# Kernel tuning notes

Measured on AMD Instinct MI355X. Metric: run time of the kernel, lower is better.

## Reference

```python
import jax, jax.numpy as jnp
import numpy as np


def _gat_layer(h, mask, w, a_src, a_dst):
    # h: [B,C,N,Fin], w: [C,H,Fin,Fout], a_*: [C,H,Fout,1], mask: [B,N,N] (True where no edge)
    h_prime = jnp.einsum('bcni,chio->bchno', h, w)          # [B,C,H,N,Fout]
    t = jnp.tanh(h_prime)
    s = jnp.einsum('bchno,cho->bchn', t, a_src[..., 0])      # src scores
    d = jnp.einsum('bchno,cho->bchn', t, a_dst[..., 0])      # dst scores
    attn = s[..., :, None] + d[..., None, :]                 # [B,C,H,N,N]
    attn = jnp.where(attn >= 0, attn, 0.2 * attn)            # leaky_relu(0.2)
    attn = jnp.where(mask[:, None, None, :, :], jnp.float32(-1e12), attn)
    attn = jax.nn.softmax(attn, axis=-1)
    return jnp.einsum('bchnm,bchmo->bchno', attn, h_prime)   # [B,C,H,N,Fout]


def setup_inputs() -> dict:
    key = jax.random.key(0)
    ks = jax.random.split(key, 8)
    B, C, N, F0, H, F = 2, 2, 1024, 64, 8, 64

    def xavier(k, shape):
        fan_in, fan_out = shape[-2], shape[-1]
        lim = (6.0 / (fan_in + fan_out)) ** 0.5
        return jax.random.uniform(k, shape, jnp.float32, -lim, lim)

    x = jax.random.normal(ks[0], (B, C, N, F0), dtype=jnp.float32)
    adj = jax.random.randint(ks[1], (B, N, N), 0, 2, dtype=jnp.int32)
    w1 = xavier(ks[2], (C, H, F0, F))
    a_src1 = xavier(ks[3], (C, H, F, 1))
    a_dst1 = xavier(ks[4], (C, H, F, 1))
    w2 = xavier(ks[5], (C, H, H * F, F))
    a_src2 = xavier(ks[6], (C, H, F, 1))
    a_dst2 = xavier(ks[7], (C, H, F, 1))
    return {"x": x, "adj": adj, "w1": w1, "a_src1": a_src1, "a_dst1": a_dst1,
            "w2": w2, "a_src2": a_src2, "a_dst2": a_dst2}


def reference(x, adj, w1, a_src1, a_dst1, w2, a_src2, a_dst2):
    B, C, N, _ = x.shape
    adj_f = adj.astype(jnp.float32) + jnp.eye(N, dtype=jnp.float32)[None]  # add self-loops
    mask = adj_f == 0                                        # [B,N,N]
    out1 = _gat_layer(x, mask, w1, a_src1, a_dst1)           # [B,C,H,N,F]
    # permute heads next to features, flatten, elu (dropout is identity in eval)
    x1 = jax.nn.elu(jnp.transpose(out1, (0, 1, 3, 2, 4)).reshape(B, C, N, -1))
    out2 = _gat_layer(x1, mask, w2, a_src2, a_dst2)          # [B,C,H,N,F]
    return out2.mean(axis=2)                                 # mean over heads -> [B,C,N,F]
```

## Files before the change

### kernel.cpp

```cpp
#include <hip/hip_runtime.h>

#define BB 2
#define CC 2
#define NN 1024
#define HH 8
#define BCHN 32
#define SVN  (BCHN*NN)
#define LOG2E 1.44269504f
#define X1S 520

typedef _Float16 f16x8 __attribute__((ext_vector_type(8)));
typedef _Float16 f16x4 __attribute__((ext_vector_type(4)));
typedef __fp16 h16x2 __attribute__((ext_vector_type(2)));
typedef float f32x4 __attribute__((ext_vector_type(4)));

__device__ __forceinline__ float fexp2(float x) {
  float r; asm("v_exp_f32 %0, %1" : "=v"(r) : "v"(x)); return r;
}


__global__ __launch_bounds__(256) void proj1_fused(
    const float* __restrict__ x, const int* __restrict__ adj,
    const float* __restrict__ w1, const float* __restrict__ w2,
    const float* __restrict__ asrc, const float* __restrict__ adst,
    _Float16* __restrict__ w2T, unsigned long long* __restrict__ bmg,
    _Float16* __restrict__ HpT, float* __restrict__ s_out, float* __restrict__ d_out)
{
  __shared__ union {
    __align__(16) _Float16 tile[64*72];
    struct { float sp[4][32]; float sd[4][32]; } pr;
  } sm;
  const int bx = blockIdx.x;
  const int t = threadIdx.x;
  const int w = t >> 6, lane = t & 63;
  const int colr = lane & 15, quad = lane >> 4;

  if (bx < 1024) {
    const int bch = bx & 31;
    const int row0 = (bx >> 5) * 32;
    const int h = bch & 7; const int bc = bch >> 3; const int c = bc & 1;

    const float* Ar0 = x + ((size_t)bc*NN + row0 + colr)*64;
    const float* Ar1 = Ar0 + (size_t)16*64;
    const float* Bw  = w1 + ((size_t)(c*HH + h))*64*64 + w*16 + colr;

    f32x4 acc0 = {0.f,0.f,0.f,0.f}, acc1 = {0.f,0.f,0.f,0.f};
    #pragma unroll
    for (int kb = 0; kb < 64; kb += 32) {
      const float4 pa0 = *(const float4*)(Ar0 + kb + quad*8);
      const float4 pa1 = *(const float4*)(Ar0 + kb + quad*8 + 4);
      const float4 pb0 = *(const float4*)(Ar1 + kb + quad*8);
      const float4 pb1 = *(const float4*)(Ar1 + kb + quad*8 + 4);
      float bv[8];
      #pragma unroll
      for (int j = 0; j < 8; ++j) bv[j] = Bw[(size_t)(kb + quad*8 + j)*64];
      f16x8 a0, a1, bf;
      a0[0]=(_Float16)pa0.x; a0[1]=(_Float16)pa0.y; a0[2]=(_Float16)pa0.z; a0[3]=(_Float16)pa0.w;
      a0[4]=(_Float16)pa1.x; a0[5]=(_Float16)pa1.y; a0[6]=(_Float16)pa1.z; a0[7]=(_Float16)pa1.w;
      a1[0]=(_Float16)pb0.x; a1[1]=(_Float16)pb0.y; a1[2]=(_Float16)pb0.z; a1[3]=(_Float16)pb0.w;
      a1[4]=(_Float16)pb1.x; a1[5]=(_Float16)pb1.y; a1[6]=(_Float16)pb1.z; a1[7]=(_Float16)pb1.w;
      #pragma unroll
      for (int j = 0; j < 8; ++j) bf[j] = (_Float16)bv[j];
      acc0 = __builtin_amdgcn_mfma_f32_16x16x32_f16(a0, bf, acc0, 0, 0, 0);
      acc1 = __builtin_amdgcn_mfma_f32_16x16x32_f16(a1, bf, acc1, 0, 0, 0);
    }

    const float af  = asrc[(c*HH + h)*64 + w*16 + colr];
    const float bf_ = adst[(c*HH + h)*64 + w*16 + colr];
    _Float16* HT = HpT + (size_t)bch*65536 + (size_t)(row0 >> 5)*2048
                       + (size_t)(w*16 + colr)*32;

    #pragma unroll
    for (int mt = 0; mt < 2; ++mt) {
      const f32x4 a = mt ? acc1 : acc0;
      f16x4 hv;
      #pragma unroll
      for (int i = 0; i < 4; ++i) {
        const float v = a[i];
        hv[i] = (_Float16)v;
        const float ex = __expf(2.f*v);
        const float th = 1.f - 2.f/(ex + 1.f);
        float ps = th * af, pd = th * bf_;
        #pragma unroll
        for (int off = 1; off < 16; off <<= 1) {
          ps += __shfl_xor(ps, off);
          pd += __shfl_xor(pd, off);
        }
        if (colr == 0) {
          sm.pr.sp[w][mt*16 + quad*4 + i] = ps;
          sm.pr.sd[w][mt*16 + quad*4 + i] = pd;
        }
      }
      *(f16x4*)(HT + mt*16 + quad*4) = hv;
    }
    __syncthreads();
    if (t < 32) {
      const float sv = sm.pr.sp[0][t] + sm.pr.sp[1][t] + sm.pr.sp[2][t] + sm.pr.sp[3][t];
      const float dv = sm.pr.sd[0][t] + sm.pr.sd[1][t] + sm.pr.sd[2][t] + sm.pr.sd[3][t];
      s_out[bch*NN + row0 + t] = sv * LOG2E;
      d_out[bch*NN + row0 + t] = dv * LOG2E;
    }
  } else if (bx < 1152) {
    const int u = bx - 1024;
    const int ch = u >> 3, k0 = (u & 7)*64;
    const float* src = w2 + ((size_t)ch*512 + k0)*64;
    #pragma unroll
    for (int j = 0; j < 4; ++j) {
      const int uu = t + j*256;
      const int k = uu >> 4, seg = uu & 15;
      const float4 v = ((const float4*)src)[(size_t)k*16 + seg];
      sm.tile[(seg*4+0)*72 + k] = (_Float16)v.x;
      sm.tile[(seg*4+1)*72 + k] = (_Float16)v.y;
      sm.tile[(seg*4+2)*72 + k] = (_Float16)v.z;
      sm.tile[(seg*4+3)*72 + k] = (_Float16)v.w;
    }
    __syncthreads();
    _Float16* dst = w2T + (size_t)ch*32768;
    #pragma unroll
    for (int j = 0; j < 2; ++j) {
      const int uu = t + j*256;
      const int f = uu >> 3, seg = uu & 7;
      const f16x8 o = *(const f16x8*)&sm.tile[f*72 + seg*8];
      const int kk = k0 + seg*8;
      *(f16x8*)(dst + (size_t)(kk >> 5)*2048 + (size_t)f*32 + (kk & 31)) = o;
    }
  } else {
    const int g = (bx - 1152)*4 + w;
    const int base = g*32;
    #pragma unroll
    for (int jb = 0; jb < 4; ++jb) {
      int vals[8];
      #pragma unroll
      for (int i = 0; i < 8; ++i) {
        const int idx = base + jb*8 + i;
        const int b = idx >> 14;
        const int n = (idx >> 4) & (NN - 1);
        const int wd = idx & 15;
        vals[i] = adj[((size_t)b*NN + n)*NN + wd*64 + lane];
      }
      #pragma unroll
      for (int i = 0; i < 8; ++i) {
        const int idx = base + jb*8 + i;
        const int n = (idx >> 4) & (NN - 1);
        const int m = (idx & 15)*64 + lane;
        const unsigned long long bits = __ballot((vals[i] != 0) || (m == n));
        if (lane == 0) bmg[idx] = bits;
      }
    }
  }
}

template<int LAYER>
__global__ __launch_bounds__(1024, 4) void attn_monster(
    const _Float16* __restrict__ HpTin, const float* __restrict__ s_arr,
    const float* __restrict__ d_arr, const unsigned long long* __restrict__ bmg,
    const _Float16* __restrict__ w2T, const float* __restrict__ asrc2,
    const float* __restrict__ adst2,
    _Float16* __restrict__ HpT2, float* __restrict__ s2, float* __restrict__ d2,
    float* __restrict__ out)
{
  __shared__ union {
    struct {
      float obuf[8][16][68];
      float dsb[8][16];
      float spb[8][16];
      float sdb[8][16];
      __align__(16) _Float16 x1[16*X1S];
    } l1;
    struct { float mbuf[16][64]; float dsb[8][16]; } l2;
  } sm;

  const int bc = blockIdx.x;
  const int r0 = blockIdx.y * 16;
  const int t = threadIdx.x;
  const int wv = t >> 6;
  const int h  = wv >> 1, kh = wv & 1;
  const int lane = t & 63;
  const int colr = lane & 15, quad = lane >> 4;
  const int bch = bc*HH + h;
  const int b = bc >> 1, c = bc & 1;

  if (LAYER == 2) sm.l2.mbuf[t >> 6][t & 63] = 0.f;
  else if (t < 256) (&sm.l1.spb[0][0])[t] = 0.f;

  const float* dg = d_arr + (size_t)bch*NN;
  const float4* dg4 = (const float4*)dg;
  float mxl = -1e30f;
  #pragma unroll
  for (int j = 0; j < 4; ++j) {
    const float4 v = dg4[lane + 64*j];
    mxl = fmaxf(fmaxf(v.x, v.y), fmaxf(fmaxf(v.z, v.w), mxl));
  }
  #pragma unroll
  for (int off = 1; off < 64; off <<= 1) mxl = fmaxf(mxl, __shfl_xor(mxl, off));
  const float maxd = mxl;

  const int r = r0 + colr;
  const float s = s_arr[(size_t)bch*NN + r];
  const float so = s + maxd;
  const float offs = fmaxf(so, 0.2f*so);
  const float sA = s - offs, sB = 0.2f*s - offs;

  unsigned long long m[8];
  {
    const unsigned long long* bm = bmg + ((size_t)b*NN + r)*16 + kh*8;
    #pragma unroll
    for (int j = 0; j < 8; ++j) m[j] = bm[j];
  }

  const _Float16* Bp = HpTin + (size_t)bch*65536 + (size_t)kh*32768 + quad*8;
  const float* dgk = dg + kh*512 + quad*8;

  f32x4 acc[4];
  f32x4 accs = {0.f,0.f,0.f,0.f};
  #pragma unroll
  for (int ft = 0; ft < 4; ++ft) acc[ft] = (f32x4){0.f,0.f,0.f,0.f};
  f16x8 ones;
  #pragma unroll
  for (int i = 0; i < 8; ++i) ones[i] = (_Float16)1.f;

  f16x8 B0[4], B1[4];
  #pragma unroll
  for (int ft = 0; ft < 4; ++ft) B0[ft] = *(const f16x8*)(Bp + (ft*16 + colr)*32);
  #pragma unroll
  for (int ft = 0; ft < 4; ++ft) B1[ft] = *(const f16x8*)(Bp + 2048 + (ft*16 + colr)*32);
  float4 dc0 = *(const float4*)(dgk),      dc1 = *(const float4*)(dgk + 4);
  float4 dn0 = *(const float4*)(dgk + 32), dn1 = *(const float4*)(dgk + 36);

  #pragma unroll
  for (int ks = 0; ks < 16; ++ks) {
    const unsigned mb = (unsigned)((m[ks >> 1] >> ((ks & 1)*32 + quad*8)) & 0xFFull);
    const float dd[8] = {dc0.x, dc0.y, dc0.z, dc0.w, dc1.x, dc1.y, dc1.z, dc1.w};
    union { f16x8 v; h16x2 hh[4]; } A;
    #pragma unroll
    for (int jp = 0; jp < 4; ++jp) {
      float p[2];
      #pragma unroll
      for (int jj = 0; jj < 2; ++jj) {
        const int j = jp*2 + jj;
        const float dj = dd[j];
        const float l = fmaxf(sA + dj, fmaf(0.2f, dj, sB));
        p[jj] = ((mb >> j) & 1u) ? fexp2(l) : 0.f;
      }
      A.hh[jp] = __builtin_amdgcn_cvt_pkrtz(p[0], p[1]);
    }
    #pragma unroll
    for (int ft = 0; ft < 4; ++ft)
      acc[ft] = __builtin_amdgcn_mfma_f32_16x16x32_f16(A.v, B0[ft], acc[ft], 0, 0, 0);
    accs = __builtin_amdgcn_mfma_f32_16x16x32_f16(A.v, ones, accs, 0, 0, 0);
    #pragma unroll
    for (int ft = 0; ft < 4; ++ft) B0[ft] = B1[ft];
    dc0 = dn0; dc1 = dn1;
    if (ks < 14) {
      #pragma unroll
      for (int ft = 0; ft < 4; ++ft)
        B1[ft] = *(const f16x8*)(Bp + (size_t)(ks+2)*2048 + (ft*16 + colr)*32);
      dn0 = *(const float4*)(dgk + (ks+2)*32);
      dn1 = *(const float4*)(dgk + (ks+2)*32 + 4);
    }
  }

  if (LAYER == 1) {
    if (kh == 0) {
      #pragma unroll
      for (int ft = 0; ft < 4; ++ft)
        #pragma unroll
        for (int i = 0; i < 4; ++i)
          sm.l1.obuf[h][quad*4 + i][ft*16 + colr] = acc[ft][i];
      if (colr == 0) {
        #pragma unroll
        for (int i = 0; i < 4; ++i) sm.l1.dsb[h][quad*4 + i] = accs[i];
      }
    }
    __syncthreads();
    if (kh == 1) {
      #pragma unroll
      for (int ft = 0; ft < 4; ++ft)
        #pragma unroll
        for (int i = 0; i < 4; ++i)
          sm.l1.obuf[h][quad*4 + i][ft*16 + colr] += acc[ft][i];
      if (colr == 0) {
        #pragma unroll
        for (int i = 0; i < 4; ++i) sm.l1.dsb[h][quad*4 + i] += accs[i];
      }
    }
    __syncthreads();
    {
      const int row = t >> 6;
      const int hp  = (t >> 3) & 7;
      const int f0  = (t & 7)*8;
      const float invd = 1.f / sm.l1.dsb[hp][row];
      const float* ob = &sm.l1.obuf[hp][row][f0];
      f16x8 xo;
      #pragma unroll
      for (int j = 0; j < 8; ++j) {
        float v = ob[j] * invd;
        v = v > 0.f ? v : expm1f(v);
        xo[j] = (_Float16)v;
      }
      *(f16x8*)&sm.l1.x1[row*X1S + hp*64 + f0] = xo;
    }
    __syncthreads();

    const int fb = kh*2;
    const _Float16* Bw = w2T + (size_t)(c*HH + h)*32768 + quad*8;
    f32x4 acc2[2];
    acc2[0] = (f32x4){0.f,0.f,0.f,0.f}; acc2[1] = (f32x4){0.f,0.f,0.f,0.f};
    f16x8 Wc[2], Wn[2];
    #pragma unroll
    for (int u = 0; u < 2; ++u) Wc[u] = *(const f16x8*)(Bw + ((fb+u)*16 + colr)*32);
    #pragma unroll
    for (int u = 0; u < 2; ++u) Wn[u] = *(const f16x8*)(Bw + 2048 + ((fb+u)*16 + colr)*32);
    #pragma unroll
    for (int k2 = 0; k2 < 16; ++k2) {
      const f16x8 Af = *(const f16x8*)&sm.l1.x1[colr*X1S + k2*32 + quad*8];
      #pragma unroll
      for (int u = 0; u < 2; ++u)
        acc2[u] = __builtin_amdgcn_mfma_f32_16x16x32_f16(Af, Wc[u], acc2[u], 0, 0, 0);
      #pragma unroll
      for (int u = 0; u < 2; ++u) Wc[u] = Wn[u];
      if (k2 < 14) {
        #pragma unroll
        for (int u = 0; u < 2; ++u)
          Wn[u] = *(const f16x8*)(Bw + (size_t)(k2+2)*2048 + ((fb+u)*16 + colr)*32);
      }
    }

    float af[2], bfv[2];
    #pragma unroll
    for (int u = 0; u < 2; ++u) {
      af[u]  = asrc2[(c*HH + h)*64 + (fb+u)*16 + colr];
      bfv[u] = adst2[(c*HH + h)*64 + (fb+u)*16 + colr];
    }
    #pragma unroll
    for (int i = 0; i < 4; ++i) {
      float ps = 0.f, pd = 0.f;
      #pragma unroll
      for (int u = 0; u < 2; ++u) {
        const float v = acc2[u][i];
        const float ex = __expf(2.f*v);
        const float th = 1.f - 2.f/(ex + 1.f);
        ps += th * af[u]; pd += th * bfv[u];
      }
      #pragma unroll
      for (int off = 1; off < 16; off <<= 1) {
        ps += __shfl_xor(ps, off);
        pd += __shfl_xor(pd, off);
      }
      if (colr == 0) {
        atomicAdd(&sm.l1.spb[h][quad*4 + i], ps);
        atomicAdd(&sm.l1.sdb[h][quad*4 + i], pd);
      }
    }
    _Float16* H2 = HpT2 + (size_t)bch*65536 + (size_t)(r0 >> 5)*2048 + (r0 & 16) + quad*4;
    #pragma unroll
    for (int u = 0; u < 2; ++u) {
      f16x4 hv;
      #pragma unroll
      for (int i = 0; i < 4; ++i) hv[i] = (_Float16)acc2[u][i];
      *(f16x4*)(H2 + ((fb+u)*16 + colr)*32) = hv;
    }
    __syncthreads();
    if (t < 128) {
      const int hp = t >> 4, rr = t & 15;
      s2[(size_t)(bc*HH + hp)*NN + r0 + rr] = sm.l1.spb[hp][rr] * LOG2E;
      d2[(size_t)(bc*HH + hp)*NN + r0 + rr] = sm.l1.sdb[hp][rr] * LOG2E;
    }
  } else {
    if (kh == 0 && colr == 0) {
      #pragma unroll
      for (int i = 0; i < 4; ++i) sm.l2.dsb[h][quad*4 + i] = accs[i];
    }
    __syncthreads();
    if (kh == 1 && colr == 0) {
      #pragma unroll
      for (int i = 0; i < 4; ++i) sm.l2.dsb[h][quad*4 + i] += accs[i];
    }
    __syncthreads();
    float inv[4];
    #pragma unroll
    for (int i = 0; i < 4; ++i) inv[i] = 0.125f / sm.l2.dsb[h][quad*4 + i];
    #pragma unroll
    for (int ft = 0; ft < 4; ++ft)
      #pragma unroll
      for (int i = 0; i < 4; ++i)
        atomicAdd(&sm.l2.mbuf[quad*4 + i][ft*16 + colr], acc[ft][i] * inv[i]);
    __syncthreads();
    out[((size_t)bc*NN + r0 + wv)*64 + lane] = sm.l2.mbuf[wv][lane];
  }
}

extern "C" void kernel_launch(void* const* d_in, const int* in_sizes, int n_in,
                              void* d_out, int out_size, void* d_ws, size_t ws_size,
                              hipStream_t stream)
{
  const float* x   = (const float*)d_in[0];
  const int*   adj = (const int*)d_in[1];
  const float* w1  = (const float*)d_in[2];
  const float* as1 = (const float*)d_in[3];
  const float* ad1 = (const float*)d_in[4];
  const float* w2  = (const float*)d_in[5];
  const float* as2 = (const float*)d_in[6];
  const float* ad2 = (const float*)d_in[7];

  char* w8 = (char*)d_ws;
  _Float16* HpT  = (_Float16*)(w8);
  _Float16* HpT2 = (_Float16*)(w8 + (4u<<20));
  _Float16* w2T  = (_Float16*)(w8 + (8u<<20));
  float* s_v  = (float*)(w8 + (10u<<20));
  float* d_v  = (float*)(w8 + (10u<<20) + SVN*4);
  float* s2_v = (float*)(w8 + (10u<<20) + SVN*8);
  float* d2_v = (float*)(w8 + (10u<<20) + SVN*12);
  unsigned long long* bmg = (unsigned long long*)(w8 + (10u<<20) + SVN*16);

  proj1_fused<<<1408, 256, 0, stream>>>(x, adj, w1, w2, as1, ad1, w2T, bmg, HpT, s_v, d_v);
  attn_monster<1><<<dim3(4, 64), 1024, 0, stream>>>(HpT, s_v, d_v, bmg, w2T, as2, ad2,
                                                    HpT2, s2_v, d2_v, (float*)d_out);
  attn_monster<2><<<dim3(4, 64), 1024, 0, stream>>>(HpT2, s2_v, d2_v, bmg, w2T, as2, ad2,
                                                    HpT2, s2_v, d2_v, (float*)d_out);
}
```

Baseline: 164.0 us.

## Stage attention and W2 operand tiles through LDS with async global_load_lds

```diff
diff --git a/kernel.cpp b/kernel.cpp
--- a/kernel.cpp
+++ b/kernel.cpp
@@ -16,6 +16,12 @@
 
 __device__ __forceinline__ float fexp2(float x) {
   float r; asm("v_exp_f32 %0, %1" : "=v"(r) : "v"(x)); return r;
+}
+
+__device__ __forceinline__ void gl_lds16(const _Float16* g, _Float16* l) {
+  __builtin_amdgcn_global_load_lds(
+      (const __attribute__((address_space(1))) void*)g,
+      (__attribute__((address_space(3))) void*)l, 16, 0, 0);
 }
 
 
@@ -160,14 +166,15 @@
     float* __restrict__ out)
 {
   __shared__ union {
+    __align__(16) _Float16 stg[2][16][2048];
     struct {
-      float obuf[8][16][68];
-      float dsb[8][16];
-      float spb[8][16];
-      float sdb[8][16];
+      float obuf[2][8][16][68];
+      float dsb[2][8][16];
+      float spb[8][16], sdb[8][16];
       __align__(16) _Float16 x1[16*X1S];
+      __align__(16) _Float16 wstg[2][16][1024];
     } l1;
-    struct { float mbuf[16][64]; float dsb[8][16]; } l2;
+    struct { float mbuf[16][64]; float dsb[2][8][16]; } l2;
   } sm;
 
   const int bc = blockIdx.x;
@@ -179,9 +186,6 @@
   const int colr = lane & 15, quad = lane >> 4;
   const int bch = bc*HH + h;
   const int b = bc >> 1, c = bc & 1;
-
-  if (LAYER == 2) sm.l2.mbuf[t >> 6][t & 63] = 0.f;
-  else if (t < 256) (&sm.l1.spb[0][0])[t] = 0.f;
 
   const float* dg = d_arr + (size_t)bch*NN;
   const float4* dg4 = (const float4*)dg;
@@ -208,7 +212,7 @@
     for (int j = 0; j < 8; ++j) m[j] = bm[j];
   }
 
-  const _Float16* Bp = HpTin + (size_t)bch*65536 + (size_t)kh*32768 + quad*8;
+  const _Float16* strip = HpTin + (size_t)bch*65536 + (size_t)kh*32768;
   const float* dgk = dg + kh*512 + quad*8;
 
   f32x4 acc[4];
@@ -219,18 +223,41 @@
   #pragma unroll
   for (int i = 0; i < 8; ++i) ones[i] = (_Float16)1.f;
 
-  f16x8 B0[4], B1[4];
-  #pragma unroll
-  for (int ft = 0; ft < 4; ++ft) B0[ft] = *(const f16x8*)(Bp + (ft*16 + colr)*32);
-  #pragma unroll
-  for (int ft = 0; ft < 4; ++ft) B1[ft] = *(const f16x8*)(Bp + 2048 + (ft*16 + colr)*32);
-  float4 dc0 = *(const float4*)(dgk),      dc1 = *(const float4*)(dgk + 4);
-  float4 dn0 = *(const float4*)(dgk + 32), dn1 = *(const float4*)(dgk + 36);
+#define STAGE_B(tt) { \
+    const _Float16* gs_ = strip + (tt)*2048 + lane*8; \
+    _Float16* ls_ = &sm.stg[(tt) & 1][wv][0]; \
+    gl_lds16(gs_,        ls_); \
+    gl_lds16(gs_ + 512,  ls_ + 512); \
+    gl_lds16(gs_ + 1024, ls_ + 1024); \
+    gl_lds16(gs_ + 1536, ls_ + 1536); }
+
+  float4 da0 = *(const float4*)(dgk);
+  float4 da1 = *(const float4*)(dgk + 4);
+  STAGE_B(0);
 
   #pragma unroll
   for (int ks = 0; ks < 16; ++ks) {
+    if (ks < 15) {
+      asm volatile("s_waitcnt lgkmcnt(0)" ::: "memory");
+      STAGE_B(ks + 1);
+      asm volatile("s_waitcnt vmcnt(4)" ::: "memory");
+    } else {
+      asm volatile("s_waitcnt vmcnt(0)" ::: "memory");
+    }
+
+    f16x8 Bc[4];
+    #pragma unroll
+    for (int ft = 0; ft < 4; ++ft)
+      Bc[ft] = *(const f16x8*)&sm.stg[ks & 1][wv][(ft*16 + colr)*32 + quad*8];
+
+    float4 na0, na1;
+    if (ks < 15) {
+      na0 = *(const float4*)(dgk + (ks+1)*32);
+      na1 = *(const float4*)(dgk + (ks+1)*32 + 4);
+    }
+
     const unsigned mb = (unsigned)((m[ks >> 1] >> ((ks & 1)*32 + quad*8)) & 0xFFull);
-    const float dd[8] = {dc0.x, dc0.y, dc0.z, dc0.w, dc1.x, dc1.y, dc1.z, dc1.w};
+    const float dd[8] = {da0.x, da0.y, da0.z, da0.w, da1.x, da1.y, da1.z, da1.w};
     union { f16x8 v; h16x2 hh[4]; } A;
     #pragma unroll
     for (int jp = 0; jp < 4; ++jp) {
@@ -246,55 +273,38 @@
     }
     #pragma unroll
     for (int ft = 0; ft < 4; ++ft)
-      acc[ft] = __builtin_amdgcn_mfma_f32_16x16x32_f16(A.v, B0[ft], acc[ft], 0, 0, 0);
+      acc[ft] = __builtin_amdgcn_mfma_f32_16x16x32_f16(A.v, Bc[ft], acc[ft], 0, 0, 0);
     accs = __builtin_amdgcn_mfma_f32_16x16x32_f16(A.v, ones, accs, 0, 0, 0);
-    #pragma unroll
-    for (int ft = 0; ft < 4; ++ft) B0[ft] = B1[ft];
-    dc0 = dn0; dc1 = dn1;
-    if (ks < 14) {
-      #pragma unroll
-      for (int ft = 0; ft < 4; ++ft)
-        B1[ft] = *(const f16x8*)(Bp + (size_t)(ks+2)*2048 + (ft*16 + colr)*32);
-      dn0 = *(const float4*)(dgk + (ks+2)*32);
-      dn1 = *(const float4*)(dgk + (ks+2)*32 + 4);
-    }
+    if (ks < 15) { da0 = na0; da1 = na1; }
   }
+#undef STAGE_B
+
+  __syncthreads();
 
   if (LAYER == 1) {
-    if (kh == 0) {
-      #pragma unroll
-      for (int ft = 0; ft < 4; ++ft)
-        #pragma unroll
-        for (int i = 0; i < 4; ++i)
-          sm.l1.obuf[h][quad*4 + i][ft*16 + colr] = acc[ft][i];
-      if (colr == 0) {
-        #pragma unroll
-        for (int i = 0; i < 4; ++i) sm.l1.dsb[h][quad*4 + i] = accs[i];
-      }
-    }
-    __syncthreads();
-    if (kh == 1) {
-      #pragma unroll
-      for (int ft = 0; ft < 4; ++ft)
-        #pragma unroll
-        for (int i = 0; i < 4; ++i)
-          sm.l1.obuf[h][quad*4 + i][ft*16 + colr] += acc[ft][i];
-      if (colr == 0) {
-        #pragma unroll
-        for (int i = 0; i < 4; ++i) sm.l1.dsb[h][quad*4 + i] += accs[i];
-      }
-    }
-    __syncthreads();
+    if (t < 256) (&sm.l1.spb[0][0])[t] = 0.f;
+    #pragma unroll
+    for (int ft = 0; ft < 4; ++ft)
+      #pragma unroll
+      for (int i = 0; i < 4; ++i)
+        sm.l1.obuf[kh][h][quad*4 + i][ft*16 + colr] = acc[ft][i];
+    if (colr == 0) {
+      #pragma unroll
+      for (int i = 0; i < 4; ++i) sm.l1.dsb[kh][h][quad*4 + i] = accs[i];
+    }
+    __syncthreads();
+
     {
       const int row = t >> 6;
       const int hp  = (t >> 3) & 7;
       const int f0  = (t & 7)*8;
-      const float invd = 1.f / sm.l1.dsb[hp][row];
-      const float* ob = &sm.l1.obuf[hp][row][f0];
+      const float invd = 1.f / (sm.l1.dsb[0][hp][row] + sm.l1.dsb[1][hp][row]);
+      const float* ob0 = &sm.l1.obuf[0][hp][row][f0];
+      const float* ob1 = &sm.l1.obuf[1][hp][row][f0];
       f16x8 xo;
       #pragma unroll
       for (int j = 0; j < 8; ++j) {
-        float v = ob[j] * invd;
+        float v = (ob0[j] + ob1[j]) * invd;
         v = v > 0.f ? v : expm1f(v);
         xo[j] = (_Float16)v;
       }
@@ -303,28 +313,36 @@
     __syncthreads();
 
     const int fb = kh*2;
-    const _Float16* Bw = w2T + (size_t)(c*HH + h)*32768 + quad*8;
+    const _Float16* wstrip = w2T + (size_t)(c*HH + h)*32768 + fb*512;
     f32x4 acc2[2];
     acc2[0] = (f32x4){0.f,0.f,0.f,0.f}; acc2[1] = (f32x4){0.f,0.f,0.f,0.f};
-    f16x8 Wc[2], Wn[2];
-    #pragma unroll
-    for (int u = 0; u < 2; ++u) Wc[u] = *(const f16x8*)(Bw + ((fb+u)*16 + colr)*32);
-    #pragma unroll
-    for (int u = 0; u < 2; ++u) Wn[u] = *(const f16x8*)(Bw + 2048 + ((fb+u)*16 + colr)*32);
+
+#define STAGE_W(tt) { \
+    const _Float16* gs_ = wstrip + (tt)*2048 + lane*8; \
+    _Float16* ls_ = &sm.l1.wstg[(tt) & 1][wv][0]; \
+    gl_lds16(gs_,       ls_); \
+    gl_lds16(gs_ + 512, ls_ + 512); }
+
+    STAGE_W(0);
     #pragma unroll
     for (int k2 = 0; k2 < 16; ++k2) {
+      if (k2 < 15) {
+        asm volatile("s_waitcnt lgkmcnt(0)" ::: "memory");
+        STAGE_W(k2 + 1);
+        asm volatile("s_waitcnt vmcnt(2)" ::: "memory");
+      } else {
+        asm volatile("s_waitcnt vmcnt(0)" ::: "memory");
+      }
+      f16x8 Wc[2];
+      #pragma unroll
+      for (int u = 0; u < 2; ++u)
+        Wc[u] = *(const f16x8*)&sm.l1.wstg[k2 & 1][wv][(u*16 + colr)*32 + quad*8];
       const f16x8 Af = *(const f16x8*)&sm.l1.x1[colr*X1S + k2*32 + quad*8];
       #pragma unroll
       for (int u = 0; u < 2; ++u)
         acc2[u] = __builtin_amdgcn_mfma_f32_16x16x32_f16(Af, Wc[u], acc2[u], 0, 0, 0);
-      #pragma unroll
-      for (int u = 0; u < 2; ++u) Wc[u] = Wn[u];
-      if (k2 < 14) {
-        #pragma unroll
-        for (int u = 0; u < 2; ++u)
-          Wn[u] = *(const f16x8*)(Bw + (size_t)(k2+2)*2048 + ((fb+u)*16 + colr)*32);
-      }
-    }
+    }
+#undef STAGE_W
 
     float af[2], bfv[2];
     #pragma unroll
@@ -367,19 +385,16 @@
       d2[(size_t)(bc*HH + hp)*NN + r0 + rr] = sm.l1.sdb[hp][rr] * LOG2E;
     }
   } else {
-    if (kh == 0 && colr == 0) {
-      #pragma unroll
-      for (int i = 0; i < 4; ++i) sm.l2.dsb[h][quad*4 + i] = accs[i];
-    }
-    __syncthreads();
-    if (kh == 1 && colr == 0) {
-      #pragma unroll
-      for (int i = 0; i < 4; ++i) sm.l2.dsb[h][quad*4 + i] += accs[i];
+    sm.l2.mbuf[t >> 6][t & 63] = 0.f;
+    if (colr == 0) {
+      #pragma unroll
+      for (int i = 0; i < 4; ++i) sm.l2.dsb[kh][h][quad*4 + i] = accs[i];
     }
     __syncthreads();
     float inv[4];
     #pragma unroll
-    for (int i = 0; i < 4; ++i) inv[i] = 0.125f / sm.l2.dsb[h][quad*4 + i];
+    for (int i = 0; i < 4; ++i)
+      inv[i] = 0.125f / (sm.l2.dsb[0][h][quad*4 + i] + sm.l2.dsb[1][h][quad*4 + i]);
     #pragma unroll
     for (int ft = 0; ft < 4; ++ft)
       #pragma unroll
```

Measured after the change: 150.8 us. 8.1% less time.
